# Kernel optimization log

Measured on AMD Instinct MI355X. Metric: run time of the kernel, lower is better.

## Reference

```python
import jax, jax.numpy as jnp
import numpy as np

POOLED_H, POOLED_W = 7, 7
SPATIAL_SCALE = 0.0625


def setup_inputs() -> dict:
    key = jax.random.key(0)
    k1, k2, k3, k4, k5, k6, k7 = jax.random.split(key, 7)
    B, C, H, W = 2, 256, 200, 272
    R = 2000
    x = jax.random.normal(k1, (B, C, H, W), dtype=jnp.float32)
    # rois: [batch_idx, cx, cy, w, h, angle_degrees] in image coordinates
    batch_idx = jax.random.randint(k2, (R,), 0, B).astype(jnp.float32)
    cx = jax.random.uniform(k3, (R,), minval=0.0, maxval=W / SPATIAL_SCALE)
    cy = jax.random.uniform(k4, (R,), minval=0.0, maxval=H / SPATIAL_SCALE)
    rw = jax.random.uniform(k5, (R,), minval=32.0, maxval=512.0)
    rh = jax.random.uniform(k6, (R,), minval=32.0, maxval=256.0)
    ang = jax.random.uniform(k7, (R,), minval=-90.0, maxval=90.0)
    rois = jnp.stack([batch_idx, cx, cy, rw, rh, ang], axis=1).astype(jnp.float32)
    return {"input": x, "rois": rois}


def _rround(x):
    # CUDA roundf (half away from zero) ~ floor(x + 0.5) for the positive range used here
    return jnp.floor(x + 0.5)


def reference(input, rois):
    B, C, H, W = input.shape
    batch_idx = rois[:, 0].astype(jnp.int32)          # [R]
    cx = rois[:, 1] * SPATIAL_SCALE
    cy = rois[:, 2] * SPATIAL_SCALE
    rw = rois[:, 3] * SPATIAL_SCALE
    rh = rois[:, 4] * SPATIAL_SCALE
    theta = rois[:, 5] * (jnp.pi / 180.0)

    # Affine transform from pooled-grid coords to feature-map coords (RRPN kernel)
    dx = -POOLED_W / 2.0
    dy = -POOLED_H / 2.0
    Sx = rw / POOLED_W
    Sy = rh / POOLED_H
    ca = jnp.cos(theta)
    sa = jnp.sin(theta)
    M00 = (ca * Sx)[:, None, None]
    M01 = (sa * Sy)[:, None, None]
    M02 = (ca * Sx * dx + sa * Sy * dy + cx)[:, None, None]
    M10 = (-sa * Sx)[:, None, None]
    M11 = (ca * Sy)[:, None, None]
    M12 = (-sa * Sx * dx + ca * Sy * dy + cy)[:, None, None]

    pw = jnp.arange(POOLED_W, dtype=rois.dtype)[None, None, :]   # [1,1,PW]
    ph = jnp.arange(POOLED_H, dtype=rois.dtype)[None, :, None]   # [1,PH,1]

    def corner(a, b):  # bin corner (pw+a, ph+b) -> feature coords, each [R,PH,PW]
        X = M00 * (pw + a) + M01 * (ph + b) + M02
        Y = M10 * (pw + a) + M11 * (ph + b) + M12
        return X, Y

    X0, Y0 = corner(0.0, 0.0)
    X1, Y1 = corner(0.0, 1.0)
    X2, Y2 = corner(1.0, 0.0)
    X3, Y3 = corner(1.0, 1.0)

    leftMost = jnp.maximum(_rround(jnp.minimum(jnp.minimum(X0, X1), jnp.minimum(X2, X3))), 0.0)
    rightMost = jnp.minimum(_rround(jnp.maximum(jnp.maximum(X0, X1), jnp.maximum(X2, X3))), W - 1.0)
    topMost = jnp.maximum(_rround(jnp.minimum(jnp.minimum(Y0, Y1), jnp.minimum(Y2, Y3))), 0.0)
    bottomMost = jnp.minimum(_rround(jnp.maximum(jnp.maximum(Y0, Y1), jnp.maximum(Y2, Y3))), H - 1.0)

    bin_cx = (leftMost + rightMost) / 2.0   # [R,PH,PW]
    bin_cy = (topMost + bottomMost) / 2.0

    bin_l = jnp.floor(bin_cx)
    bin_r = jnp.ceil(bin_cx)
    bin_t = jnp.floor(bin_cy)
    bin_b = jnp.ceil(bin_cy)

    rx = bin_cx - jnp.floor(bin_cx)
    ry = bin_cy - jnp.floor(bin_cy)
    wlt = (1.0 - rx) * (1.0 - ry)
    wrt = rx * (1.0 - ry)
    wrb = rx * ry
    wlb = (1.0 - rx) * ry

    bidx = batch_idx[:, None, None]  # [R,1,1]

    def sample(yy, xx):
        # masked gather of input[b, :, y, x] -> [R,PH,PW,C]
        m = ((yy > -1.0) & (yy < H) & (xx > -1.0) & (xx < W)).astype(input.dtype)
        yi = jnp.clip(yy.astype(jnp.int32), 0, H - 1)
        xi = jnp.clip(xx.astype(jnp.int32), 0, W - 1)
        v = input[bidx, :, yi, xi]  # advanced idx -> [R,PH,PW,C]
        return v * m[..., None]

    lt = sample(bin_t, bin_l)
    rt = sample(bin_t, bin_r)
    lb = sample(bin_b, bin_l)
    rb = sample(bin_b, bin_r)

    out = (lt * wlt[..., None] + rt * wrt[..., None]
           + rb * wrb[..., None] + lb * wlb[..., None])   # [R,PH,PW,C]
    return jnp.transpose(out, (0, 3, 1, 2))                 # [R,C,PH,PW]
```

## Files before the change

### kernel.cpp

```cpp
#include <hip/hip_runtime.h>
#include <math.h>

#define B_   2
#define C_   256
#define H_   200
#define W_   272
#define HW_  (H_*W_)
#define NBIN 49
#define SCALE 0.0625f

typedef float v4f __attribute__((ext_vector_type(4)));

__device__ __forceinline__ unsigned short f2bf(float f) {
    union { float f; unsigned int i; } v; v.f = f;
    unsigned int x = v.i;
    return (unsigned short)((x + 0x7FFFu + ((x >> 16) & 1u)) >> 16);
}
__device__ __forceinline__ float bf2f(unsigned int u16) {
    union { unsigned int i; float f; } v; v.i = u16 << 16; return v.f;
}

__device__ __forceinline__ float edge_mask(float yy, float xx) {
    return (yy > -1.0f && yy < (float)H_ && xx > -1.0f && xx < (float)W_) ? 1.0f : 0.0f;
}

__device__ void compute_geom(const float* __restrict__ rois, int r, int bin,
                             int& b, int& yt, int& yb, int& xl, int& xr,
                             float w[4]) {
#pragma clang fp contract(off)
    const float* rp = rois + r * 6;
    b = (int)rp[0];
    float cx = rp[1] * SCALE;
    float cy = rp[2] * SCALE;
    float rw = rp[3] * SCALE;
    float rh = rp[4] * SCALE;
    float theta = rp[5] * (float)(M_PI / 180.0);
    float Sx = rw / 7.0f;
    float Sy = rh / 7.0f;
    double th = (double)theta;
    float ca = (float)cos(th);
    float sa = (float)sin(th);

    float M00 = ca * Sx;
    float M01 = sa * Sy;
    float M02 = (M00 * (-3.5f) + M01 * (-3.5f)) + cx;
    float M10 = (-sa) * Sx;
    float M11 = ca * Sy;
    float M12 = (M10 * (-3.5f) + M11 * (-3.5f)) + cy;

    float pwf = (float)(bin % 7);
    float phf = (float)(bin / 7);
    float x0 = pwf, x1 = pwf + 1.0f;
    float y0 = phf, y1 = phf + 1.0f;

    float X00 = (M00 * x0 + M01 * y0) + M02;
    float X01 = (M00 * x0 + M01 * y1) + M02;
    float X10 = (M00 * x1 + M01 * y0) + M02;
    float X11 = (M00 * x1 + M01 * y1) + M02;
    float Y00 = (M10 * x0 + M11 * y0) + M12;
    float Y01 = (M10 * x0 + M11 * y1) + M12;
    float Y10 = (M10 * x1 + M11 * y0) + M12;
    float Y11 = (M10 * x1 + M11 * y1) + M12;

    float minX = fminf(fminf(X00, X01), fminf(X10, X11));
    float maxX = fmaxf(fmaxf(X00, X01), fmaxf(X10, X11));
    float minY = fminf(fminf(Y00, Y01), fminf(Y10, Y11));
    float maxY = fmaxf(fmaxf(Y00, Y01), fmaxf(Y10, Y11));

    float leftMost   = fmaxf(floorf(minX + 0.5f), 0.0f);
    float rightMost  = fminf(floorf(maxX + 0.5f), (float)(W_ - 1));
    float topMost    = fmaxf(floorf(minY + 0.5f), 0.0f);
    float bottomMost = fminf(floorf(maxY + 0.5f), (float)(H_ - 1));

    float bcx = (leftMost + rightMost) * 0.5f;
    float bcy = (topMost + bottomMost) * 0.5f;
    float fl = floorf(bcx), fr = ceilf(bcx);
    float ft = floorf(bcy), fb = ceilf(bcy);
    float rx = bcx - fl;
    float ry = bcy - ft;

    float wlt = (1.0f - rx) * (1.0f - ry);
    float wrt = rx * (1.0f - ry);
    float wrb = rx * ry;
    float wlb = (1.0f - rx) * ry;

    w[0] = wlt * edge_mask(ft, fl);
    w[1] = wrt * edge_mask(ft, fr);
    w[2] = wlb * edge_mask(fb, fl);
    w[3] = wrb * edge_mask(fb, fr);

    yt = min(max((int)ft, 0), H_ - 1);
    yb = min(max((int)fb, 0), H_ - 1);
    xl = min(max((int)fl, 0), W_ - 1);
    xr = min(max((int)fr, 0), W_ - 1);
}

__global__ __launch_bounds__(256) void transpose_geom(const float* __restrict__ in,
                                                      unsigned short* __restrict__ xt,
                                                      unsigned int* __restrict__ geom,
                                                      const float* __restrict__ rois,
                                                      int R) {
    if (blockIdx.y == 4) {
        int total = R * NBIN;
        for (int gid = (blockIdx.z * 850 + blockIdx.x) * 256 + threadIdx.x;
             gid < total; gid += 1700 * 256) {
            int r = gid / NBIN, bin = gid - r * NBIN;
            int b, yt, yb, xl, xr; float w[4];
            compute_geom(rois, r, bin, b, yt, yb, xl, xr, w);
            int base = b * HW_ * C_;
            uint4 o, wu;
            o.x = base + (yt * W_ + xl) * C_;
            o.y = base + (yt * W_ + xr) * C_;
            o.z = base + (yb * W_ + xl) * C_;
            o.w = base + (yb * W_ + xr) * C_;
            wu.x = __float_as_uint(w[0]);
            wu.y = __float_as_uint(w[1]);
            wu.z = __float_as_uint(w[2]);
            wu.w = __float_as_uint(w[3]);
            uint4* gp = (uint4*)(geom + (size_t)gid * 8);
            gp[0] = o;
            gp[1] = wu;
        }
        return;
    }

    __shared__ float tile[64][65];
    int b  = blockIdx.z;
    int p0 = blockIdx.x * 64;
    int c0 = blockIdx.y * 64;
    const float*    ib = in + (size_t)b * C_ * HW_;
    unsigned short* ob = xt + (size_t)b * HW_ * C_;
    int t = threadIdx.x;

    {
        int col4 = t & 15;
        int row  = t >> 4;
        #pragma unroll
        for (int k = 0; k < 4; k++) {
            int c = row + k * 16;
            float4 v = *(const float4*)(ib + (size_t)(c0 + c) * HW_ + p0 + col4 * 4);
            int p = col4 * 4;
            tile[p + 0][c] = v.x;
            tile[p + 1][c] = v.y;
            tile[p + 2][c] = v.z;
            tile[p + 3][c] = v.w;
        }
    }
    __syncthreads();
    {
        int c8 = t & 7;
        int pr = t >> 3;
        #pragma unroll
        for (int k = 0; k < 2; k++) {
            int p = pr + k * 32;
            ushort4 lo, hi;
            const float* tp = &tile[p][c8 * 8];
            lo.x = f2bf(tp[0]); lo.y = f2bf(tp[1]); lo.z = f2bf(tp[2]); lo.w = f2bf(tp[3]);
            hi.x = f2bf(tp[4]); hi.y = f2bf(tp[5]); hi.z = f2bf(tp[6]); hi.w = f2bf(tp[7]);
            unsigned short* dst = ob + (size_t)(p0 + p) * C_ + c0 + c8 * 8;
            *(ushort4*)(dst)     = lo;
            *(ushort4*)(dst + 4) = hi;
        }
    }
}

__device__ __forceinline__ void bilerp4(uint2 lt, uint2 rt, uint2 lb, uint2 rb,
                                        float w0, float w1, float w2, float w3,
                                        float acc[4]) {
#pragma clang fp contract(off)
    float a0 = bf2f(lt.x & 0xFFFFu), a1 = bf2f(lt.x >> 16),
          a2 = bf2f(lt.y & 0xFFFFu), a3 = bf2f(lt.y >> 16);
    float b0 = bf2f(rt.x & 0xFFFFu), b1 = bf2f(rt.x >> 16),
          b2 = bf2f(rt.y & 0xFFFFu), b3 = bf2f(rt.y >> 16);
    float c0v = bf2f(lb.x & 0xFFFFu), c1v = bf2f(lb.x >> 16),
          c2v = bf2f(lb.y & 0xFFFFu), c3v = bf2f(lb.y >> 16);
    float d0 = bf2f(rb.x & 0xFFFFu), d1 = bf2f(rb.x >> 16),
          d2 = bf2f(rb.y & 0xFFFFu), d3 = bf2f(rb.y >> 16);
    acc[0] = ((w0 * a0 + w1 * b0) + w3 * d0) + w2 * c0v;
    acc[1] = ((w0 * a1 + w1 * b1) + w3 * d1) + w2 * c1v;
    acc[2] = ((w0 * a2 + w1 * b2) + w3 * d2) + w2 * c2v;
    acc[3] = ((w0 * a3 + w1 * b3) + w3 * d3) + w2 * c3v;
}

__global__ __launch_bounds__(256) void rroi_main_bf16(const unsigned short* __restrict__ xt,
                                                      const unsigned int* __restrict__ geom,
                                                      float* __restrict__ outp) {
    __shared__ unsigned short lout[C_ * NBIN];

    int r    = blockIdx.x;
    int tid  = threadIdx.x;
    int lane = tid & 63;
    int wv   = tid >> 6;
    int c4   = lane * 4;

    const uint4* gb = (const uint4*)(geom + (size_t)r * NBIN * 8);

    for (int b0 = wv; b0 < NBIN; b0 += 8) {
        int b1 = b0 + 4;
        uint4 go0 = gb[2 * b0];
        uint4 gu0 = gb[2 * b0 + 1];
        if (b1 < NBIN) {
            uint4 go1 = gb[2 * b1];
            uint4 gu1 = gb[2 * b1 + 1];
            uint2 lt0 = *(const uint2*)(xt + go0.x + c4);
            uint2 rt0 = *(const uint2*)(xt + go0.y + c4);
            uint2 lb0 = *(const uint2*)(xt + go0.z + c4);
            uint2 rb0 = *(const uint2*)(xt + go0.w + c4);
            uint2 lt1 = *(const uint2*)(xt + go1.x + c4);
            uint2 rt1 = *(const uint2*)(xt + go1.y + c4);
            uint2 lb1 = *(const uint2*)(xt + go1.z + c4);
            uint2 rb1 = *(const uint2*)(xt + go1.w + c4);
            float acc0[4], acc1[4];
            bilerp4(lt0, rt0, lb0, rb0,
                    __uint_as_float(gu0.x), __uint_as_float(gu0.y),
                    __uint_as_float(gu0.z), __uint_as_float(gu0.w), acc0);
            bilerp4(lt1, rt1, lb1, rb1,
                    __uint_as_float(gu1.x), __uint_as_float(gu1.y),
                    __uint_as_float(gu1.z), __uint_as_float(gu1.w), acc1);
            #pragma unroll
            for (int jj = 0; jj < 4; jj++) {
                int j = (jj + (lane >> 3)) & 3;
                float v0 = (j == 0) ? acc0[0] : (j == 1) ? acc0[1] : (j == 2) ? acc0[2] : acc0[3];
                float v1 = (j == 0) ? acc1[0] : (j == 1) ? acc1[1] : (j == 2) ? acc1[2] : acc1[3];
                lout[(c4 + j) * NBIN + b0] = f2bf(v0);
                lout[(c4 + j) * NBIN + b1] = f2bf(v1);
            }
        } else {
            uint2 lt0 = *(const uint2*)(xt + go0.x + c4);
            uint2 rt0 = *(const uint2*)(xt + go0.y + c4);
            uint2 lb0 = *(const uint2*)(xt + go0.z + c4);
            uint2 rb0 = *(const uint2*)(xt + go0.w + c4);
            float acc0[4];
            bilerp4(lt0, rt0, lb0, rb0,
                    __uint_as_float(gu0.x), __uint_as_float(gu0.y),
                    __uint_as_float(gu0.z), __uint_as_float(gu0.w), acc0);
            #pragma unroll
            for (int jj = 0; jj < 4; jj++) {
                int j = (jj + (lane >> 3)) & 3;
                float v0 = (j == 0) ? acc0[0] : (j == 1) ? acc0[1] : (j == 2) ? acc0[2] : acc0[3];
                lout[(c4 + j) * NBIN + b0] = f2bf(v0);
            }
        }
    }
    __syncthreads();

    const unsigned int* lu = (const unsigned int*)lout;
    float* obase = outp + (size_t)r * (C_ * NBIN);
    const int n4 = (C_ * NBIN) / 4;
    for (int f = tid; f < n4; f += 256) {
        uint2 u = *(const uint2*)(&lu[2 * f]);
        v4f v;
        v.x = bf2f(u.x & 0xFFFFu); v.y = bf2f(u.x >> 16);
        v.z = bf2f(u.y & 0xFFFFu); v.w = bf2f(u.y >> 16);
        __builtin_nontemporal_store(v, (v4f*)(obase + 4 * f));
    }
}

__global__ __launch_bounds__(256) void rroi_main_direct(const float* __restrict__ x,
                                                        const float* __restrict__ rois,
                                                        float* __restrict__ outp) {
    __shared__ float loutf[C_ * NBIN];
    __shared__ int   goff[NBIN][4];
    __shared__ float gw[NBIN][4];

    int r = blockIdx.x;
    int tid = threadIdx.x;

    if (tid < NBIN) {
        int b, yt, yb, xl, xr; float w[4];
        compute_geom(rois, r, tid, b, yt, yb, xl, xr, w);
        int base = b * C_ * HW_;
        goff[tid][0] = base + yt * W_ + xl;
        goff[tid][1] = base + yt * W_ + xr;
        goff[tid][2] = base + yb * W_ + xl;
        goff[tid][3] = base + yb * W_ + xr;
        gw[tid][0] = w[0]; gw[tid][1] = w[1]; gw[tid][2] = w[2]; gw[tid][3] = w[3];
    }
    __syncthreads();

    int c = tid;
    int coff = c * HW_;
    for (int bin = 0; bin < NBIN; bin++) {
        float w0 = gw[bin][0], w1 = gw[bin][1], w2 = gw[bin][2], w3 = gw[bin][3];
        float lt = x[goff[bin][0] + coff];
        float rt = x[goff[bin][1] + coff];
        float lb = x[goff[bin][2] + coff];
        float rb = x[goff[bin][3] + coff];
        float v;
        {
#pragma clang fp contract(off)
            v = ((w0 * lt + w1 * rt) + w3 * rb) + w2 * lb;
        }
        loutf[c * NBIN + bin] = v;
    }
    __syncthreads();

    float* o = outp + (size_t)r * (C_ * NBIN);
    const int n4 = (C_ * NBIN) / 4;
    for (int i = tid; i < n4; i += 256)
        *(float4*)(o + i * 4) = *(const float4*)(&loutf[i * 4]);
}

extern "C" void kernel_launch(void* const* d_in, const int* in_sizes, int n_in,
                              void* d_out, int out_size, void* d_ws, size_t ws_size,
                              hipStream_t stream) {
    const float* x    = (const float*)d_in[0];
    const float* rois = (const float*)d_in[1];
    float*       outp = (float*)d_out;
    int R = in_sizes[1] / 6;

    size_t geom_off = 64ull * 1024 * 1024;
    size_t need = geom_off + (size_t)R * NBIN * 8 * sizeof(unsigned int);
    if (ws_size >= need) {
        unsigned short* xt   = (unsigned short*)d_ws;
        unsigned int*   geom = (unsigned int*)((char*)d_ws + geom_off);
        dim3 g(HW_ / 64, 5, B_);
        transpose_geom<<<g, 256, 0, stream>>>(x, xt, geom, rois, R);
        rroi_main_bf16<<<R, 256, 0, stream>>>(xt, geom, outp);
    } else {
        rroi_main_direct<<<R, 256, 0, stream>>>(x, rois, outp);
    }
}
```

Before: 61.89 us.

## Split pipeline by batch to overlap batch-1 transpose with batch-0 ROI pooling

The single transpose+geometry kernel and the ROI kernel become three launches. The first transposes batch 0 and computes geometry. The second transposes batch 1 while pooling the batch-0 ROIs. The third pools the batch-1 ROIs. The goal is to hide the batch-1 transpose behind the batch-0 gather work, at the cost of an extra launch and ROI blocks that exit early after reading geometry.

```diff
diff --git a/kernel.cpp b/kernel.cpp
--- a/kernel.cpp
+++ b/kernel.cpp
@@ -95,43 +95,12 @@
     xr = min(max((int)fr, 0), W_ - 1);
 }
 
-__global__ __launch_bounds__(256) void transpose_geom(const float* __restrict__ in,
-                                                      unsigned short* __restrict__ xt,
-                                                      unsigned int* __restrict__ geom,
-                                                      const float* __restrict__ rois,
-                                                      int R) {
-    if (blockIdx.y == 4) {
-        int total = R * NBIN;
-        for (int gid = (blockIdx.z * 850 + blockIdx.x) * 256 + threadIdx.x;
-             gid < total; gid += 1700 * 256) {
-            int r = gid / NBIN, bin = gid - r * NBIN;
-            int b, yt, yb, xl, xr; float w[4];
-            compute_geom(rois, r, bin, b, yt, yb, xl, xr, w);
-            int base = b * HW_ * C_;
-            uint4 o, wu;
-            o.x = base + (yt * W_ + xl) * C_;
-            o.y = base + (yt * W_ + xr) * C_;
-            o.z = base + (yb * W_ + xl) * C_;
-            o.w = base + (yb * W_ + xr) * C_;
-            wu.x = __float_as_uint(w[0]);
-            wu.y = __float_as_uint(w[1]);
-            wu.z = __float_as_uint(w[2]);
-            wu.w = __float_as_uint(w[3]);
-            uint4* gp = (uint4*)(geom + (size_t)gid * 8);
-            gp[0] = o;
-            gp[1] = wu;
-        }
-        return;
-    }
-
-    __shared__ float tile[64][65];
-    int b  = blockIdx.z;
-    int p0 = blockIdx.x * 64;
-    int c0 = blockIdx.y * 64;
+__device__ __forceinline__ void transpose_tile(const float* __restrict__ in,
+                                               unsigned short* __restrict__ xt,
+                                               int b, int p0, int c0, int t,
+                                               float (*tile)[65]) {
     const float*    ib = in + (size_t)b * C_ * HW_;
     unsigned short* ob = xt + (size_t)b * HW_ * C_;
-    int t = threadIdx.x;
-
     {
         int col4 = t & 15;
         int row  = t >> 4;
@@ -182,13 +151,10 @@
     acc[3] = ((w0 * a3 + w1 * b3) + w3 * d3) + w2 * c3v;
 }
 
-__global__ __launch_bounds__(256) void rroi_main_bf16(const unsigned short* __restrict__ xt,
-                                                      const unsigned int* __restrict__ geom,
-                                                      float* __restrict__ outp) {
-    __shared__ unsigned short lout[C_ * NBIN];
-
-    int r    = blockIdx.x;
-    int tid  = threadIdx.x;
+__device__ __forceinline__ void main_roi(const unsigned short* __restrict__ xt,
+                                         const unsigned int* __restrict__ geom,
+                                         float* __restrict__ outp, int r, int tid,
+                                         unsigned short* lout) {
     int lane = tid & 63;
     int wv   = tid >> 6;
     int c4   = lane * 4;
@@ -256,6 +222,68 @@
     }
 }
 
+#define SM_BYTES 25088
+
+__global__ __launch_bounds__(256) void k1_t0_geom(const float* __restrict__ in,
+                                                  unsigned short* __restrict__ xt,
+                                                  unsigned int* __restrict__ geom,
+                                                  const float* __restrict__ rois,
+                                                  int R) {
+    __shared__ __align__(16) char sm[SM_BYTES];
+    int id = blockIdx.x;
+    if (id < 3400) {
+        transpose_tile(in, xt, 0, (id % 850) * 64, (id / 850) * 64,
+                       threadIdx.x, (float(*)[65])sm);
+        return;
+    }
+    int total = R * NBIN;
+    for (int gid = (id - 3400) * 256 + threadIdx.x; gid < total; gid += 1700 * 256) {
+        int r = gid / NBIN, bin = gid - r * NBIN;
+        int b, yt, yb, xl, xr; float w[4];
+        compute_geom(rois, r, bin, b, yt, yb, xl, xr, w);
+        int base = b * HW_ * C_;
+        uint4 o, wu;
+        o.x = base + (yt * W_ + xl) * C_;
+        o.y = base + (yt * W_ + xr) * C_;
+        o.z = base + (yb * W_ + xl) * C_;
+        o.w = base + (yb * W_ + xr) * C_;
+        wu.x = __float_as_uint(w[0]);
+        wu.y = __float_as_uint(w[1]);
+        wu.z = __float_as_uint(w[2]);
+        wu.w = __float_as_uint(w[3]);
+        uint4* gp = (uint4*)(geom + (size_t)gid * 8);
+        gp[0] = o;
+        gp[1] = wu;
+    }
+}
+
+__global__ __launch_bounds__(256) void k2_t1_main0(const float* __restrict__ in,
+                                                   unsigned short* __restrict__ xt,
+                                                   const unsigned int* __restrict__ geom,
+                                                   float* __restrict__ outp,
+                                                   int R) {
+    __shared__ __align__(16) char sm[SM_BYTES];
+    int id = blockIdx.x;
+    if (id < 3400) {
+        transpose_tile(in, xt, 1, (id % 850) * 64, (id / 850) * 64,
+                       threadIdx.x, (float(*)[65])sm);
+        return;
+    }
+    int r = id - 3400;
+    if (r >= R) return;
+    if (geom[(size_t)r * NBIN * 8] >= (unsigned int)(HW_ * C_)) return;
+    main_roi(xt, geom, outp, r, threadIdx.x, (unsigned short*)sm);
+}
+
+__global__ __launch_bounds__(256) void k3_main1(const unsigned short* __restrict__ xt,
+                                                const unsigned int* __restrict__ geom,
+                                                float* __restrict__ outp) {
+    __shared__ __align__(16) char sm[SM_BYTES];
+    int r = blockIdx.x;
+    if (geom[(size_t)r * NBIN * 8] < (unsigned int)(HW_ * C_)) return;
+    main_roi(xt, geom, outp, r, threadIdx.x, (unsigned short*)sm);
+}
+
 __global__ __launch_bounds__(256) void rroi_main_direct(const float* __restrict__ x,
                                                         const float* __restrict__ rois,
                                                         float* __restrict__ outp) {
@@ -314,9 +342,9 @@
     if (ws_size >= need) {
         unsigned short* xt   = (unsigned short*)d_ws;
         unsigned int*   geom = (unsigned int*)((char*)d_ws + geom_off);
-        dim3 g(HW_ / 64, 5, B_);
-        transpose_geom<<<g, 256, 0, stream>>>(x, xt, geom, rois, R);
-        rroi_main_bf16<<<R, 256, 0, stream>>>(xt, geom, outp);
+        k1_t0_geom<<<5100, 256, 0, stream>>>(x, xt, geom, rois, R);
+        k2_t1_main0<<<3400 + R, 256, 0, stream>>>(x, xt, geom, outp, R);
+        k3_main1<<<R, 256, 0, stream>>>(xt, geom, outp);
     } else {
         rroi_main_direct<<<R, 256, 0, stream>>>(x, rois, outp);
     }
```

Result: slower. 71.10 us (+14.9%).
